# Kernel optimization log

Hardware: AMD Instinct MI355X
Metric: run time of the kernel (lower is better)

Reference implementation:

```python
import jax, jax.numpy as jnp
import numpy as np

N_NODES = 50000
N_EDGES = 800000
D = 128


def gin_layer(x, edge_index, edge_attr, ee1, ee2, W1, b1, W2, b2):
    # PyG default flow source_to_target: x_j = x[edge_index[0]], aggregate at edge_index[1]
    src, dst = edge_index[0], edge_index[1]
    edge_emb = ee1[edge_attr[:, 0]] + ee2[edge_attr[:, 1]]           # [E, D]
    msg = x[src] + edge_emb                                          # [E, D]
    aggr = jax.ops.segment_sum(msg, dst, num_segments=x.shape[0])    # [N, D]
    h = jax.nn.relu(aggr @ W1 + b1)                                  # [N, 2D]
    return h @ W2 + b2                                               # [N, out]


def setup_inputs() -> dict:
    key = jax.random.key(0)
    ks = jax.random.split(key, 16)
    s = 1.0 / np.sqrt(D)
    inp = {
        "x": jax.random.normal(ks[0], (N_NODES, D), jnp.float32),
        "edge_index": jax.random.randint(ks[1], (2, N_EDGES), 0, N_NODES, dtype=jnp.int32),
        "edge_attr": jax.random.randint(ks[2], (N_EDGES, 2), 0, 3, dtype=jnp.int32),
        "ee1_0": jax.random.normal(ks[3], (6, D), jnp.float32) * s,
        "ee2_0": jax.random.normal(ks[4], (3, D), jnp.float32) * s,
        "W1_0": jax.random.normal(ks[5], (D, 2 * D), jnp.float32) * s,
        "b1_0": jnp.zeros((2 * D,), jnp.float32),
        "W2_0": jax.random.normal(ks[6], (2 * D, D), jnp.float32) * s,
        "b2_0": jnp.zeros((D,), jnp.float32),
        "ee1_1": jax.random.normal(ks[7], (6, D), jnp.float32) * s,
        "ee2_1": jax.random.normal(ks[8], (3, D), jnp.float32) * s,
        "W1_1": jax.random.normal(ks[9], (D, 2 * D), jnp.float32) * s,
        "b1_1": jnp.zeros((2 * D,), jnp.float32),
        "W2_1": jax.random.normal(ks[10], (2 * D, D), jnp.float32) * s,
        "b2_1": jnp.zeros((D,), jnp.float32),
    }
    return inp


def reference(x, edge_index, edge_attr, ee1_0, ee2_0, W1_0, b1_0, W2_0, b2_0,
              ee1_1, ee2_1, W1_1, b1_1, W2_1, b2_1):
    h = gin_layer(x, edge_index, edge_attr, ee1_0, ee2_0, W1_0, b1_0, W2_0, b2_0)
    h = jax.nn.relu(h)  # activation between GNN layers
    out = gin_layer(h, edge_index, edge_attr, ee1_1, ee2_1, W1_1, b1_1, W2_1, b2_1)
    return out  # jk='last'
```

## Files before the change

### kernel.cpp

```cpp
#include <hip/hip_runtime.h>

typedef __attribute__((ext_vector_type(8))) short s16x8;
typedef __attribute__((ext_vector_type(4))) float f32x4;
typedef unsigned short u16;
typedef unsigned char u8;
typedef unsigned long long u64;

#define D_FEAT 128
#define TILE1 4096

__device__ __forceinline__ u16 f2bf(float f) {
    unsigned u = __builtin_bit_cast(unsigned, f);
    u = u + 0x7fffu + ((u >> 16) & 1u);
    return (u16)(u >> 16);
}

__global__ __launch_bounds__(256) void tobf16_kernel(const float4* __restrict__ X,
                                                     u16* __restrict__ out, int n4) {
    int i = blockIdx.x * 256 + threadIdx.x;
    if (i < n4) {
        float4 v = X[i];
        uint2 p;
        p.x = (unsigned)f2bf(v.x) | ((unsigned)f2bf(v.y) << 16);
        p.y = (unsigned)f2bf(v.z) | ((unsigned)f2bf(v.w) << 16);
        *(uint2*)(out + (size_t)i * 4) = p;
    }
}

__global__ __launch_bounds__(256) void hist1_kernel(const int* __restrict__ dst,
                                                    int* __restrict__ ghist,
                                                    int E, int nb1, int bins) {
    __shared__ int h[256];
    const int t = threadIdx.x;
    h[t] = 0;
    __syncthreads();
    const int base = blockIdx.x * TILE1;
    #pragma unroll
    for (int j = 0; j < TILE1 / 256; ++j) {
        int e = base + j * 256 + t;
        if (e < E) atomicAdd(&h[dst[e] >> 8], 1);
    }
    __syncthreads();
    if (t < bins) ghist[t * nb1 + blockIdx.x] = h[t];
}

__global__ __launch_bounds__(256) void scan1a_kernel(int* __restrict__ ghist,
                                                     int* __restrict__ btot, int nb1) {
    __shared__ int wt[4];
    const int t = threadIdx.x, lane = t & 63, wid = t >> 6;
    const int bin = blockIdx.x;
    const int v = (t < nb1) ? ghist[bin * nb1 + t] : 0;
    int s = v;
    #pragma unroll
    for (int off = 1; off < 64; off <<= 1) {
        int u = __shfl_up(s, off, 64);
        if (lane >= off) s += u;
    }
    if (lane == 63) wt[wid] = s;
    __syncthreads();
    int add = 0;
    #pragma unroll
    for (int w = 0; w < 4; ++w) add += (w < wid) ? wt[w] : 0;
    s += add;
    if (t < nb1) ghist[bin * nb1 + t] = s - v;
    if (t == 255) btot[bin] = s;
}

__global__ __launch_bounds__(256) void scan1b_kernel(const int* __restrict__ btot,
                                                     int* __restrict__ bbase,
                                                     int* __restrict__ row_start, int bins) {
    __shared__ int wt[4];
    const int t = threadIdx.x, lane = t & 63, wid = t >> 6;
    const int v = (t < bins) ? btot[t] : 0;
    int s = v;
    #pragma unroll
    for (int off = 1; off < 64; off <<= 1) {
        int u = __shfl_up(s, off, 64);
        if (lane >= off) s += u;
    }
    if (lane == 63) wt[wid] = s;
    __syncthreads();
    int add = 0;
    #pragma unroll
    for (int w = 0; w < 4; ++w) add += (w < wid) ? wt[w] : 0;
    s += add;
    if (t < bins) bbase[t] = s - v;
    if (t == 255) bbase[bins] = s;
    if (t == 0) row_start[0] = 0;
}

__global__ __launch_bounds__(256) void scatter1_kernel(const int* __restrict__ src,
                                                       const int* __restrict__ dst,
                                                       const int* __restrict__ eattr,
                                                       const int* __restrict__ ghist,
                                                       const int* __restrict__ bbase,
                                                       u64* __restrict__ buf1,
                                                       int E, int nb1, int bins) {
    __shared__ int lofs[256];
    const int t = threadIdx.x;
    if (t < bins) lofs[t] = bbase[t] + ghist[t * nb1 + blockIdx.x];
    __syncthreads();
    const int base = blockIdx.x * TILE1;
    #pragma unroll
    for (int j = 0; j < TILE1 / 256; ++j) {
        int e = base + j * 256 + t;
        if (e < E) {
            int d = dst[e];
            int2 at = ((const int2*)eattr)[e];
            unsigned pay = (unsigned)src[e] | ((unsigned)(at.x * 3 + at.y) << 16);
            int pos = atomicAdd(&lofs[d >> 8], 1);
            buf1[pos] = ((u64)(unsigned)d << 32) | pay;
        }
    }
}

__global__ __launch_bounds__(256) void bucket2_kernel(const u64* __restrict__ buf1,
                                                      const int* __restrict__ bbase,
                                                      int* __restrict__ row_start,
                                                      unsigned* __restrict__ edges, int N) {
    __shared__ int cnt[256];
    __shared__ int cur[256];
    __shared__ int wt[4];
    const int t = threadIdx.x, lane = t & 63, wid = t >> 6;
    const int bin = blockIdx.x;
    const int lo = bbase[bin], hi = bbase[bin + 1];
    cnt[t] = 0;
    __syncthreads();
    for (int i = lo + t; i < hi; i += 256)
        atomicAdd(&cnt[(int)(buf1[i] >> 32) & 255], 1);
    __syncthreads();
    const int v = cnt[t];
    int s = v;
    #pragma unroll
    for (int off = 1; off < 64; off <<= 1) {
        int u = __shfl_up(s, off, 64);
        if (lane >= off) s += u;
    }
    if (lane == 63) wt[wid] = s;
    __syncthreads();
    int add = 0;
    #pragma unroll
    for (int w = 0; w < 4; ++w) add += (w < wid) ? wt[w] : 0;
    const int incl = s + add;
    const int g = bin * 256 + t;
    if (g < N) row_start[g + 1] = lo + incl;
    cur[t] = incl - v;
    __syncthreads();
    for (int i = lo + t; i < hi; i += 256) {
        u64 rec = buf1[i];
        int loc = atomicAdd(&cur[(int)(rec >> 32) & 255], 1);
        edges[lo + loc] = (unsigned)rec;
    }
}

__global__ __launch_bounds__(256) void transpose_kernel(const float* __restrict__ W1_0,
                                                        const float* __restrict__ W2_0,
                                                        const float* __restrict__ W1_1,
                                                        const float* __restrict__ W2_1,
                                                        u16* __restrict__ out) {
    int mat = blockIdx.y;
    const float* s = (mat == 0) ? W1_0 : (mat == 1) ? W2_0 : (mat == 2) ? W1_1 : W2_1;
    int K = (mat & 1) ? 256 : 128;
    int Nc = 384 - K;
    u16* d = out + mat * 32768;
    int idx = blockIdx.x * 256 + threadIdx.x;
    int n = idx / K, k = idx - n * K;
    d[idx] = f2bf(s[k * Nc + n]);
}

__global__ __launch_bounds__(128) void emb_kernel(const float* __restrict__ ee1_0,
                                                  const float* __restrict__ ee2_0,
                                                  const float* __restrict__ ee1_1,
                                                  const float* __restrict__ ee2_1,
                                                  float* __restrict__ emb) {
    int code = blockIdx.x;
    int layer = blockIdx.y;
    int d = threadIdx.x;
    int a0 = code / 3, a1 = code - a0 * 3;
    const float* e1 = layer ? ee1_1 : ee1_0;
    const float* e2 = layer ? ee2_1 : ee2_0;
    emb[layer * 18 * 128 + code * 128 + d] = e1[a0 * 128 + d] + e2[a1 * 128 + d];
}

__global__ __launch_bounds__(256) void aggregate_kernel(const u16* __restrict__ X,
                                                        const int* __restrict__ row_start,
                                                        const unsigned* __restrict__ edges,
                                                        const float* __restrict__ emb,
                                                        u16* __restrict__ A, int N) {
    __shared__ float semb[18 * 128];
    for (int i = threadIdx.x; i < 18 * 128; i += 256) semb[i] = emb[i];
    __syncthreads();
    const int node = blockIdx.x * 4 + (threadIdx.x >> 6);
    const int lane = threadIdx.x & 63;
    if (node >= N) return;
    int s = __builtin_amdgcn_readfirstlane(row_start[node]);
    const int e = __builtin_amdgcn_readfirstlane(row_start[node + 1]);
    const float2* sem2 = (const float2*)semb;
    float a0 = 0.f, a1 = 0.f;

    while (s < e) {
        const int take = (e - s < 64) ? (e - s) : 64;
        unsigned pl = edges[s + (lane < take ? lane : 0)];
        #pragma unroll
        for (int c = 0; c < 4; ++c) {
            const int cb = c * 16;
            if (cb + 16 <= take) {
                unsigned ps[16];
                unsigned xv[16];
                float2 ev[16];
                #pragma unroll
                for (int j = 0; j < 16; ++j)
                    ps[j] = __builtin_amdgcn_readlane(pl, cb + j);
                #pragma unroll
                for (int j = 0; j < 16; ++j)
                    xv[j] = *(const unsigned*)(X + (ps[j] & 0xFFFFu) * D_FEAT + lane * 2);
                #pragma unroll
                for (int j = 0; j < 16; ++j)
                    ev[j] = sem2[(int)(ps[j] >> 16) * 64 + lane];
                #pragma unroll
                for (int j = 0; j < 16; ++j) {
                    a0 += __builtin_bit_cast(float, xv[j] << 16) + ev[j].x;
                    a1 += __builtin_bit_cast(float, xv[j] & 0xFFFF0000u) + ev[j].y;
                }
            } else if (cb < take) {
                unsigned ps[16];
                unsigned xv[16];
                float2 ev[16];
                #pragma unroll
                for (int j = 0; j < 16; ++j)
                    ps[j] = __builtin_amdgcn_readlane(pl, cb + j);
                #pragma unroll
                for (int j = 0; j < 16; ++j)
                    xv[j] = *(const unsigned*)(X + (ps[j] & 0xFFFFu) * D_FEAT + lane * 2);
                #pragma unroll
                for (int j = 0; j < 16; ++j)
                    ev[j] = sem2[(int)(ps[j] >> 16) * 64 + lane];
                #pragma unroll
                for (int j = 0; j < 16; ++j) {
                    const float m = (cb + j < take) ? 1.f : 0.f;
                    a0 += m * (__builtin_bit_cast(float, xv[j] << 16) + ev[j].x);
                    a1 += m * (__builtin_bit_cast(float, xv[j] & 0xFFFF0000u) + ev[j].y);
                }
            }
        }
        s += take;
    }
    unsigned outp = (unsigned)f2bf(a0) | ((unsigned)f2bf(a1) << 16);
    *(unsigned*)(A + node * D_FEAT + lane * 2) = outp;
}

template <bool RELU2, bool OUTF32>
__global__ __launch_bounds__(256, 1) void mlp_kernel(const u16* __restrict__ A,
                                                     const u16* __restrict__ B1t,
                                                     const float* __restrict__ bias1,
                                                     const u16* __restrict__ B2t,
                                                     const float* __restrict__ bias2,
                                                     void* __restrict__ C, int M, int nt) {
    extern __shared__ __align__(16) u16 lds[];
    u16* w1 = lds;
    u16* w2 = lds + 32768;
    u16* hh = lds + 65536;
    const int tid = threadIdx.x;
    const int wave = tid >> 6;
    const int lane = tid & 63;
    const int m16 = lane & 15;
    const int quad = lane >> 4;

    {
        const uint4* src1 = (const uint4*)B1t;
        const uint4* src2 = (const uint4*)B2t;
        #pragma unroll
        for (int i = 0; i < 16; ++i) {
            int s = i * 256 + tid;
            uint4 v = src1[s];
            int c = (((s >> 8) * 4 + ((s >> 2) & 3)) << 6) | ((s & 3) << 4) | ((s >> 4) & 15);
            *(uint4*)(w1 + c * 8) = v;
        }
        #pragma unroll
        for (int i = 0; i < 16; ++i) {
            int s = i * 256 + tid;
            uint4 v = src2[s];
            int c = (((s >> 9) * 8 + ((s >> 2) & 7)) << 6) | ((s & 3) << 4) | ((s >> 5) & 15);
            *(uint4*)(w2 + c * 8) = v;
        }
    }
    float b1v[16];
    #pragma unroll
    for (int t = 0; t < 16; ++t) b1v[t] = bias1[t * 16 + m16];
    float b2v[8];
    #pragma unroll
    for (int t = 0; t < 8; ++t) b2v[t] = bias2[t * 16 + m16];

    const int hbase = wave * 4096;

    int tile = blockIdx.x;
    s16x8 af[4];
    #pragma unroll
    for (int kb = 0; kb < 4; ++kb) af[kb] = s16x8{};
    if (tile < nt) {
        const int arow = tile * 64 + wave * 16 + m16;
        if (arow < M) {
            #pragma unroll
            for (int kb = 0; kb < 4; ++kb)
                af[kb] = *(const s16x8*)(A + (size_t)arow * 128 + kb * 32 + quad * 8);
        }
    }

    __syncthreads();

    for (; tile < nt; tile += 256) {
        const int row0 = tile * 64 + wave * 16;

        f32x4 acc[16];
        #pragma unroll
        for (int t = 0; t < 16; ++t) acc[t] = f32x4{0, 0, 0, 0};
        #pragma unroll
        for (int kb = 0; kb < 4; ++kb) {
            #pragma unroll
            for (int t = 0; t < 16; ++t) {
                s16x8 bf = *(const s16x8*)(w1 + (((((t << 2) | kb) << 6) | lane) * 8));
                acc[t] = __builtin_amdgcn_mfma_f32_16x16x32_bf16(af[kb], bf, acc[t], 0, 0, 0);
            }
        }

        const int ntile = tile + 256;
        s16x8 afn[4];
        #pragma unroll
        for (int kb = 0; kb < 4; ++kb) afn[kb] = s16x8{};
        if (ntile < nt) {
            const int arow = ntile * 64 + wave * 16 + m16;
            if (arow < M) {
                #pragma unroll
                for (int kb = 0; kb < 4; ++kb)
                    afn[kb] = *(const s16x8*)(A + (size_t)arow * 128 + kb * 32 + quad * 8);
            }
        }

        #pragma unroll
        for (int t = 0; t < 16; ++t) {
            const int col = t * 16 + m16;
            #pragma unroll
            for (int r = 0; r < 4; ++r) {
                const int row = quad * 4 + r;
                float v = acc[t][r] + b1v[t];
                v = v > 0.f ? v : 0.f;
                hh[(hbase + row * 256 + col) ^ ((row & 7) << 3)] = f2bf(v);
            }
        }
        __syncthreads();

        f32x4 acc2[8];
        #pragma unroll
        for (int t = 0; t < 8; ++t) acc2[t] = f32x4{0, 0, 0, 0};
        #pragma unroll
        for (int kb = 0; kb < 8; ++kb) {
            s16x8 haf = *(const s16x8*)(hh + ((hbase + m16 * 256 + kb * 32 + quad * 8) ^ ((m16 & 7) << 3)));
            #pragma unroll
            for (int t = 0; t < 8; ++t) {
                s16x8 bf = *(const s16x8*)(w2 + (((((t << 3) | kb) << 6) | lane) * 8));
                acc2[t] = __builtin_amdgcn_mfma_f32_16x16x32_bf16(haf, bf, acc2[t], 0, 0, 0);
            }
        }

        #pragma unroll
        for (int t = 0; t < 8; ++t) {
            const int col = t * 16 + m16;
            #pragma unroll
            for (int r = 0; r < 4; ++r) {
                const int row = row0 + quad * 4 + r;
                if (row < M) {
                    float v = acc2[t][r] + b2v[t];
                    if (RELU2) v = v > 0.f ? v : 0.f;
                    if (OUTF32) ((float*)C)[(size_t)row * 128 + col] = v;
                    else        ((u16*)C)[(size_t)row * 128 + col] = f2bf(v);
                }
            }
        }
        __syncthreads();

        #pragma unroll
        for (int kb = 0; kb < 4; ++kb) af[kb] = afn[kb];
    }
}

extern "C" void kernel_launch(void* const* d_in, const int* in_sizes, int n_in,
                              void* d_out, int out_size, void* d_ws, size_t ws_size,
                              hipStream_t stream) {
    const int N = in_sizes[0] / D_FEAT;
    const int E = in_sizes[1] / 2;

    const float* x    = (const float*)d_in[0];
    const int* eidx   = (const int*)d_in[1];
    const int* eattr  = (const int*)d_in[2];
    const float* ee1_0 = (const float*)d_in[3];
    const float* ee2_0 = (const float*)d_in[4];
    const float* W1_0  = (const float*)d_in[5];
    const float* b1_0  = (const float*)d_in[6];
    const float* W2_0  = (const float*)d_in[7];
    const float* b2_0  = (const float*)d_in[8];
    const float* ee1_1 = (const float*)d_in[9];
    const float* ee2_1 = (const float*)d_in[10];
    const float* W1_1  = (const float*)d_in[11];
    const float* b1_1  = (const float*)d_in[12];
    const float* W2_1  = (const float*)d_in[13];
    const float* b2_1  = (const float*)d_in[14];

    const int nb1  = (E + TILE1 - 1) / TILE1;
    const int bins = (N + 255) / 256;

    char* ws = (char*)d_ws;
    size_t off = 0;
    auto alloc = [&](size_t bytes) { size_t o = off; off = (off + bytes + 255) & ~(size_t)255; return o; };
    size_t o_rowstart = alloc((size_t)(N + 1) * 4);
    size_t o_edges    = alloc((size_t)E * 4);
    size_t o_ghist    = alloc((size_t)bins * nb1 * 4);
    size_t o_base     = alloc((size_t)(bins + 1) * 4);
    size_t o_btot     = alloc((size_t)bins * 4);
    size_t o_emb      = alloc(2 * 18 * 128 * 4);
    size_t o_wt       = alloc(4 * 32768 * 2);
    size_t o_aa       = alloc((size_t)N * D_FEAT * 2);

    int*      row_start = (int*)(ws + o_rowstart);
    unsigned* edges     = (unsigned*)(ws + o_edges);
    int*      ghist     = (int*)(ws + o_ghist);
    int*      bbase     = (int*)(ws + o_base);
    int*      btot      = (int*)(ws + o_btot);
    float*    emb       = (float*)(ws + o_emb);
    u16*      W1t_0     = (u16*)(ws + o_wt);
    u16*      W2t_0     = W1t_0 + 32768;
    u16*      W1t_1     = W2t_0 + 32768;
    u16*      W2t_1     = W1t_1 + 32768;
    u16*      AA        = (u16*)(ws + o_aa);
    u64*      buf1      = (u64*)(ws + o_aa);

    u16* X2 = (u16*)d_out;
    u16* xb = (u16*)d_out + (size_t)N * D_FEAT;

    const int nt = (N + 63) / 64;
    const int aggB = (N + 3) / 4;
    const int n4 = N * D_FEAT / 4;
    const int LDS_MLP = 163840;

    static bool attr_done = false;
    if (!attr_done) {
        hipFuncSetAttribute((const void*)mlp_kernel<true, false>,
                            hipFuncAttributeMaxDynamicSharedMemorySize, LDS_MLP);
        hipFuncSetAttribute((const void*)mlp_kernel<false, true>,
                            hipFuncAttributeMaxDynamicSharedMemorySize, LDS_MLP);
        attr_done = true;
    }

    tobf16_kernel<<<(n4 + 255) / 256, 256, 0, stream>>>((const float4*)x, xb, n4);

    hist1_kernel<<<nb1, 256, 0, stream>>>(eidx + E, ghist, E, nb1, bins);
    scan1a_kernel<<<bins, 256, 0, stream>>>(ghist, btot, nb1);
    scan1b_kernel<<<1, 256, 0, stream>>>(btot, bbase, row_start, bins);
    scatter1_kernel<<<nb1, 256, 0, stream>>>(eidx, eidx + E, eattr, ghist, bbase, buf1, E, nb1, bins);
    bucket2_kernel<<<bins, 256, 0, stream>>>(buf1, bbase, row_start, edges, N);

    emb_kernel<<<dim3(18, 2), 128, 0, stream>>>(ee1_0, ee2_0, ee1_1, ee2_1, emb);
    transpose_kernel<<<dim3(128, 4), 256, 0, stream>>>(W1_0, W2_0, W1_1, W2_1, W1t_0);

    aggregate_kernel<<<aggB, 256, 0, stream>>>(xb, row_start, edges, emb, AA, N);
    mlp_kernel<true, false><<<256, 256, LDS_MLP, stream>>>(AA, W1t_0, b1_0, W2t_0, b2_0, X2, N, nt);

    aggregate_kernel<<<aggB, 256, 0, stream>>>(X2, row_start, edges, emb + 18 * 128, AA, N);
    mlp_kernel<false, true><<<256, 256, LDS_MLP, stream>>>(AA, W1t_1, b1_1, W2t_1, b2_1, d_out, N, nt);
}
```

Baseline: 278.9 us.

## Replace per-edge embedding adds with per-node edge-type count histograms

The bucket pass now counts, for each destination node, how many incoming edges carry each of the 18 edge-attribute codes, and packs these counts into five 32-bit words per node as 8-bit fields. Both aggregate passes then sum only the gathered source features per edge and add the embedding once per code, weighted by its count. This removes one LDS read and two adds per edge per lane. In exchange the bucket kernel uses an extra 18 KB of shared memory and does an extra atomic per edge, and the 8-bit count fields overflow if a node has more than 255 edges of one code.

```diff
diff --git a/kernel.cpp b/kernel.cpp
--- a/kernel.cpp
+++ b/kernel.cpp
@@ -117,14 +117,17 @@
 __global__ __launch_bounds__(256) void bucket2_kernel(const u64* __restrict__ buf1,
                                                       const int* __restrict__ bbase,
                                                       int* __restrict__ row_start,
-                                                      unsigned* __restrict__ edges, int N) {
+                                                      unsigned* __restrict__ edges,
+                                                      unsigned* __restrict__ countsw, int N) {
     __shared__ int cnt[256];
     __shared__ int cur[256];
     __shared__ int wt[4];
+    __shared__ unsigned ccnt[256 * 18];
     const int t = threadIdx.x, lane = t & 63, wid = t >> 6;
     const int bin = blockIdx.x;
     const int lo = bbase[bin], hi = bbase[bin + 1];
     cnt[t] = 0;
+    for (int i = t; i < 256 * 18; i += 256) ccnt[i] = 0;
     __syncthreads();
     for (int i = lo + t; i < hi; i += 256)
         atomicAdd(&cnt[(int)(buf1[i] >> 32) & 255], 1);
@@ -148,8 +151,20 @@
     __syncthreads();
     for (int i = lo + t; i < hi; i += 256) {
         u64 rec = buf1[i];
-        int loc = atomicAdd(&cur[(int)(rec >> 32) & 255], 1);
+        const int local = (int)(rec >> 32) & 255;
+        int loc = atomicAdd(&cur[local], 1);
         edges[lo + loc] = (unsigned)rec;
+        atomicAdd(&ccnt[local * 18 + ((unsigned)rec >> 16)], 1);
+    }
+    __syncthreads();
+    if (g < N) {
+        unsigned w[5] = {0, 0, 0, 0, 0};
+        #pragma unroll
+        for (int c = 0; c < 18; ++c)
+            w[c >> 2] |= ccnt[t * 18 + c] << (8 * (c & 3));
+        #pragma unroll
+        for (int k = 0; k < 5; ++k)
+            countsw[(size_t)g * 5 + k] = w[k];
     }
 }
 
@@ -186,6 +201,7 @@
                                                         const int* __restrict__ row_start,
                                                         const unsigned* __restrict__ edges,
                                                         const float* __restrict__ emb,
+                                                        const unsigned* __restrict__ countsw,
                                                         u16* __restrict__ A, int N) {
     __shared__ float semb[18 * 128];
     for (int i = threadIdx.x; i < 18 * 128; i += 256) semb[i] = emb[i];
@@ -193,6 +209,11 @@
     const int node = blockIdx.x * 4 + (threadIdx.x >> 6);
     const int lane = threadIdx.x & 63;
     if (node >= N) return;
+
+    unsigned cw[5];
+    #pragma unroll
+    for (int k = 0; k < 5; ++k) cw[k] = countsw[(size_t)node * 5 + k];
+
     int s = __builtin_amdgcn_readfirstlane(row_start[node]);
     const int e = __builtin_amdgcn_readfirstlane(row_start[node + 1]);
     const float2* sem2 = (const float2*)semb;
@@ -204,10 +225,9 @@
         #pragma unroll
         for (int c = 0; c < 4; ++c) {
             const int cb = c * 16;
-            if (cb + 16 <= take) {
+            if (cb < take) {
                 unsigned ps[16];
                 unsigned xv[16];
-                float2 ev[16];
                 #pragma unroll
                 for (int j = 0; j < 16; ++j)
                     ps[j] = __builtin_amdgcn_readlane(pl, cb + j);
@@ -215,36 +235,30 @@
                 for (int j = 0; j < 16; ++j)
                     xv[j] = *(const unsigned*)(X + (ps[j] & 0xFFFFu) * D_FEAT + lane * 2);
                 #pragma unroll
-                for (int j = 0; j < 16; ++j)
-                    ev[j] = sem2[(int)(ps[j] >> 16) * 64 + lane];
-                #pragma unroll
-                for (int j = 0; j < 16; ++j) {
-                    a0 += __builtin_bit_cast(float, xv[j] << 16) + ev[j].x;
-                    a1 += __builtin_bit_cast(float, xv[j] & 0xFFFF0000u) + ev[j].y;
-                }
-            } else if (cb < take) {
-                unsigned ps[16];
-                unsigned xv[16];
-                float2 ev[16];
-                #pragma unroll
-                for (int j = 0; j < 16; ++j)
-                    ps[j] = __builtin_amdgcn_readlane(pl, cb + j);
-                #pragma unroll
-                for (int j = 0; j < 16; ++j)
-                    xv[j] = *(const unsigned*)(X + (ps[j] & 0xFFFFu) * D_FEAT + lane * 2);
-                #pragma unroll
-                for (int j = 0; j < 16; ++j)
-                    ev[j] = sem2[(int)(ps[j] >> 16) * 64 + lane];
-                #pragma unroll
                 for (int j = 0; j < 16; ++j) {
                     const float m = (cb + j < take) ? 1.f : 0.f;
-                    a0 += m * (__builtin_bit_cast(float, xv[j] << 16) + ev[j].x);
-                    a1 += m * (__builtin_bit_cast(float, xv[j] & 0xFFFF0000u) + ev[j].y);
+                    a0 += m * __builtin_bit_cast(float, xv[j] << 16);
+                    a1 += m * __builtin_bit_cast(float, xv[j] & 0xFFFF0000u);
                 }
             }
         }
         s += take;
     }
+
+    #pragma unroll
+    for (int w = 0; w < 5; ++w) {
+        #pragma unroll
+        for (int b = 0; b < 4; ++b) {
+            const int code = w * 4 + b;
+            if (code < 18) {
+                const float cf = (float)((cw[w] >> (8 * b)) & 255u);
+                float2 ev = sem2[code * 64 + lane];
+                a0 += cf * ev.x;
+                a1 += cf * ev.y;
+            }
+        }
+    }
+
     unsigned outp = (unsigned)f2bf(a0) | ((unsigned)f2bf(a1) << 16);
     *(unsigned*)(A + node * D_FEAT + lane * 2) = outp;
 }
@@ -416,6 +430,7 @@
     size_t o_ghist    = alloc((size_t)bins * nb1 * 4);
     size_t o_base     = alloc((size_t)(bins + 1) * 4);
     size_t o_btot     = alloc((size_t)bins * 4);
+    size_t o_counts   = alloc((size_t)N * 20);
     size_t o_emb      = alloc(2 * 18 * 128 * 4);
     size_t o_wt       = alloc(4 * 32768 * 2);
     size_t o_aa       = alloc((size_t)N * D_FEAT * 2);
@@ -425,6 +440,7 @@
     int*      ghist     = (int*)(ws + o_ghist);
     int*      bbase     = (int*)(ws + o_base);
     int*      btot      = (int*)(ws + o_btot);
+    unsigned* countsw   = (unsigned*)(ws + o_counts);
     float*    emb       = (float*)(ws + o_emb);
     u16*      W1t_0     = (u16*)(ws + o_wt);
     u16*      W2t_0     = W1t_0 + 32768;
@@ -456,14 +472,14 @@
     scan1a_kernel<<<bins, 256, 0, stream>>>(ghist, btot, nb1);
     scan1b_kernel<<<1, 256, 0, stream>>>(btot, bbase, row_start, bins);
     scatter1_kernel<<<nb1, 256, 0, stream>>>(eidx, eidx + E, eattr, ghist, bbase, buf1, E, nb1, bins);
-    bucket2_kernel<<<bins, 256, 0, stream>>>(buf1, bbase, row_start, edges, N);
+    bucket2_kernel<<<bins, 256, 0, stream>>>(buf1, bbase, row_start, edges, countsw, N);
 
     emb_kernel<<<dim3(18, 2), 128, 0, stream>>>(ee1_0, ee2_0, ee1_1, ee2_1, emb);
     transpose_kernel<<<dim3(128, 4), 256, 0, stream>>>(W1_0, W2_0, W1_1, W2_1, W1t_0);
 
-    aggregate_kernel<<<aggB, 256, 0, stream>>>(xb, row_start, edges, emb, AA, N);
+    aggregate_kernel<<<aggB, 256, 0, stream>>>(xb, row_start, edges, emb, countsw, AA, N);
     mlp_kernel<true, false><<<256, 256, LDS_MLP, stream>>>(AA, W1t_0, b1_0, W2t_0, b2_0, X2, N, nt);
 
-    aggregate_kernel<<<aggB, 256, 0, stream>>>(X2, row_start, edges, emb + 18 * 128, AA, N);
+    aggregate_kernel<<<aggB, 256, 0, stream>>>(X2, row_start, edges, emb + 18 * 128, countsw, AA, N);
     mlp_kernel<false, true><<<256, 256, LDS_MLP, stream>>>(AA, W1t_1, b1_1, W2t_1, b2_1, d_out, N, nt);
 }
```

Result: no change. 275.7 us (-1.1%).
